# Kernel optimization log

Hardware: AMD Instinct MI355X
Metric: run time of the kernel (lower is better)

## Reference

```python
import jax, jax.numpy as jnp
import numpy as np

M = 28            # mask head resolution (mask_logit[i] is MxM)
NUM_CLASSES = 80  # max value of cls_idx (mask_image channel count)


def setup_inputs() -> dict:
    key = jax.random.key(0)
    k1, k2, k3, k4, k5, k6, k7 = jax.random.split(key, 7)
    N, H, W = 100, 800, 800
    cx = jax.random.uniform(k1, (N,), minval=0.0, maxval=float(W - 1))
    cy = jax.random.uniform(k2, (N,), minval=0.0, maxval=float(H - 1))
    bw = jax.random.uniform(k3, (N,), minval=20.0, maxval=300.0)
    bh = jax.random.uniform(k4, (N,), minval=20.0, maxval=300.0)
    mask_rois = jnp.stack([cx - bw / 2, cy - bh / 2, cx + bw / 2, cy + bh / 2], axis=1).astype(jnp.float32)
    cls_prob = jax.random.uniform(k5, (N,), dtype=jnp.float32)
    mask_prob = jax.random.normal(k6, (N, M, M), dtype=jnp.float32)
    cls_idx = jax.random.randint(k7, (N,), 1, NUM_CLASSES + 1, dtype=jnp.int32)
    return {"mask_rois": mask_rois, "cls_prob": cls_prob, "mask_prob": mask_prob,
            "cls_idx": cls_idx, "im_h": H, "im_w": W}


def _paste(logit, box, H, W):
    """Bilinear-paste an MxM logit into the full HxW image (== cv2.resize to (w,h)
    then placing at the box, evaluated directly on image pixel coords)."""
    x0, y0, x1, y1 = box[0], box[1], box[2], box[3]  # int32
    w = jnp.maximum(x1 - x0 + 1, 1).astype(jnp.float32)
    h = jnp.maximum(y1 - y0 + 1, 1).astype(jnp.float32)
    xs = jnp.arange(W, dtype=jnp.float32)
    ys = jnp.arange(H, dtype=jnp.float32)
    # cv2 bilinear mapping: src = (dst + 0.5) * (M / size) - 0.5, clamped at borders
    sx = jnp.clip((xs - x0.astype(jnp.float32) + 0.5) * (M / w) - 0.5, 0.0, M - 1.0)
    sy = jnp.clip((ys - y0.astype(jnp.float32) + 0.5) * (M / h) - 0.5, 0.0, M - 1.0)
    ix0 = jnp.floor(sx).astype(jnp.int32); ix1 = jnp.minimum(ix0 + 1, M - 1); fx = sx - ix0
    iy0 = jnp.floor(sy).astype(jnp.int32); iy1 = jnp.minimum(iy0 + 1, M - 1); fy = sy - iy0
    v00 = logit[iy0[:, None], ix0[None, :]]
    v01 = logit[iy0[:, None], ix1[None, :]]
    v10 = logit[iy1[:, None], ix0[None, :]]
    v11 = logit[iy1[:, None], ix1[None, :]]
    val = ((1 - fy)[:, None] * ((1 - fx)[None, :] * v00 + fx[None, :] * v01)
           + fy[:, None] * ((1 - fx)[None, :] * v10 + fx[None, :] * v11))
    xi = jnp.arange(W, dtype=jnp.int32)
    yi = jnp.arange(H, dtype=jnp.int32)
    inside_x = (xi >= jnp.maximum(x0, 0)) & (xi < jnp.minimum(x1 + 1, W))
    inside_y = (yi >= jnp.maximum(y0, 0)) & (yi < jnp.minimum(y1 + 1, H))
    inside = inside_y[:, None] & inside_x[None, :]
    return jnp.where(inside, val, 0.0), inside


def _forward(mask_rois, cls_prob, mask_prob, cls_idx, H, W, thr):
    N = mask_prob.shape[0]
    order = jnp.argsort(-cls_prob)                       # sort by score, descending
    boxes = mask_rois[order].astype(jnp.int32)
    logits = mask_prob[order]
    cls = cls_idx[order].astype(jnp.int32) - 1           # 0-based class ids
    pasted, inside = jax.vmap(lambda l, b: _paste(l, b, H, W))(logits, boxes)  # [N,H,W]

    def step(mask_image, xs):
        logit, ins, c = xs
        mask = (logit > 0) & ins                          # thresholded, in-image crop mask
        prev = mask_image[c]
        msum = jnp.sum(mask).astype(jnp.float32)
        ovl = jnp.sum(mask & prev).astype(jnp.float32)    # overlap with accumulated class mask
        keep = (msum > 0) & (ovl <= thr * msum)           # skip if ratio > threshold
        mask_image = mask_image.at[c].set(prev | (mask & keep))
        return mask_image, keep

    mask_image0 = jnp.zeros((NUM_CLASSES, H, W), dtype=bool)
    _, keep = jax.lax.scan(step, mask_image0, (pasted, inside, cls))

    # compact kept masks to the front (frame_id order); dropped boxes go to slot N (discarded)
    pos = jnp.where(keep, jnp.cumsum(keep.astype(jnp.int32)) - 1, N)
    energy = jnp.where(inside & keep[:, None, None], pasted, 0.0)
    full = jnp.zeros((N + 1, H, W), pasted.dtype).at[pos].set(energy)
    mask_energy = full[:N][None]                          # [1, N, H, W], kept masks first
    keep_inds = jnp.full((N + 1,), -1, jnp.int32).at[pos].set(
        jnp.where(keep, order.astype(jnp.int32), -1))[:N]
    return keep_inds, mask_energy


def reference(mask_rois, cls_prob, mask_prob, cls_idx, im_h, im_w):
    return _forward(mask_rois, cls_prob, mask_prob, cls_idx, int(im_h), int(im_w), 0.3)
```

## Files before the change

kernel.cpp:

```cpp
#include <hip/hip_runtime.h>

#define NINST 100
#define MLOG 28
#define IMG 800
#define LOGSZ (MLOG * MLOG)

#define OFF_ORDER 0
#define OFF_CLS   100
#define OFF_BOX   200
#define OFF_MSUM  600
#define OFF_SLOT  800
#define OFF_NK    900
#define OFF_MASK  1024
#define ROWW      12
#define MSTRIDE   (ROWW * 304)
#define PCAP      256
#define F4TOT     (NINST * IMG * IMG / 4)
#define NZBLK     (F4TOT / 256)

__global__ __launch_bounds__(256) void k_mask_zero(const float* __restrict__ mask_prob,
                                                   const float* __restrict__ cls_prob,
                                                   const float* __restrict__ rois,
                                                   const int* __restrict__ cls_idx,
                                                   int* __restrict__ ws,
                                                   float* __restrict__ out) {
    int b = blockIdx.x, tid = threadIdx.x;
    if (b >= NINST) {
        size_t pi = (size_t)(b - NINST) * 256 + tid;
        ((float4*)(out + NINST))[pi] = make_float4(0.f, 0.f, 0.f, 0.f);
        return;
    }
    __shared__ float s_p[NINST];
    __shared__ int s_order[NINST];
    __shared__ float lg[LOGSZ];
    __shared__ int red[256];
    if (tid < NINST) s_p[tid] = cls_prob[tid];
    __syncthreads();
    if (tid < NINST) {
        float p = s_p[tid];
        int r = 0;
        for (int j = 0; j < NINST; j++) {
            float q = s_p[j];
            r += (q > p) || (q == p && j < tid);
        }
        s_order[r] = tid;
    }
    __syncthreads();
    int n = b;
    int orig = s_order[n];
    int x0 = (int)rois[4 * orig], y0 = (int)rois[4 * orig + 1];
    int x1 = (int)rois[4 * orig + 2], y1 = (int)rois[4 * orig + 3];
    if (b == 0 && tid < NINST) {
        int o = s_order[tid];
        ws[OFF_ORDER + tid] = o;
        ws[OFF_CLS + tid] = cls_idx[o] - 1;
#pragma unroll
        for (int k = 0; k < 4; k++)
            ws[OFF_BOX + 4 * tid + k] = (int)rois[4 * o + k];
    }
    for (int i = tid; i < LOGSZ; i += 256) lg[i] = mask_prob[orig * LOGSZ + i];
    __syncthreads();
    int xs = max(x0, 0), xe = min(x1 + 1, IMG);
    int ys = max(y0, 0), ye = min(y1 + 1, IMG);
    int wx0 = xs >> 5, nw = ((xe + 31) >> 5) - wx0, nrows = ye - ys;
    float wf = fmaxf((float)(x1 - x0 + 1), 1.f), hf = fmaxf((float)(y1 - y0 + 1), 1.f);
    float rx = 28.f / wf, ry = 28.f / hf;
    unsigned* mb = (unsigned*)(ws + OFF_MASK) + n * MSTRIDE;
    int total = nrows * nw, cnt = 0;
    for (int t = tid; t < total; t += 256) {
        int row = t / nw, wc = t - row * nw;
        int y = ys + row;
        float sy = ((float)y - (float)y0 + 0.5f) * ry - 0.5f;
        sy = fminf(fmaxf(sy, 0.f), 27.f);
        int iy0 = (int)sy, iy1 = min(iy0 + 1, 27);
        float fy = sy - (float)iy0;
        const float* r0 = lg + iy0 * MLOG;
        const float* r1 = lg + iy1 * MLOG;
        unsigned bits = 0u;
        int xbase = (wx0 + wc) << 5;
        int j0 = max(xs - xbase, 0), j1 = min(xe - xbase, 32);
        for (int j = j0; j < j1; j++) {
            int xx = xbase + j;
            float sx = ((float)xx - (float)x0 + 0.5f) * rx - 0.5f;
            sx = fminf(fmaxf(sx, 0.f), 27.f);
            int ix0 = (int)sx, ix1 = min(ix0 + 1, 27);
            float fx = sx - (float)ix0;
            float val = (1.f - fy) * ((1.f - fx) * r0[ix0] + fx * r0[ix1]) +
                        fy * ((1.f - fx) * r1[ix0] + fx * r1[ix1]);
            bits |= (val > 0.f) ? (1u << j) : 0u;
        }
        mb[row * ROWW + wc] = bits;
        cnt += __popc(bits);
    }
    red[tid] = cnt;
    __syncthreads();
    for (int s = 128; s; s >>= 1) {
        if (tid < s) red[tid] += red[tid + s];
        __syncthreads();
    }
    if (tid == 0) ws[OFF_MSUM + n] = red[0];
}

__device__ __forceinline__ bool box_ovl(const int* sb, int a, int b2) {
    int axs = max(sb[4 * a], 0), axe = min(sb[4 * a + 2] + 1, IMG);
    int ays = max(sb[4 * a + 1], 0), aye = min(sb[4 * a + 3] + 1, IMG);
    int bxs = max(sb[4 * b2], 0), bxe = min(sb[4 * b2 + 2] + 1, IMG);
    int bys = max(sb[4 * b2 + 1], 0), bye = min(sb[4 * b2 + 3] + 1, IMG);
    return axs < bxe && bxs < axe && ays < bye && bys < aye;
}

__global__ __launch_bounds__(64) void k_scan64(int* __restrict__ ws, float* __restrict__ out) {
    int ln = threadIdx.x;
    __shared__ int s_cls[NINST], s_msum[NINST], s_box[4 * NINST];
    __shared__ int s_pi[PCAP], s_pj[PCAP], s_po[PCAP];
    __shared__ int s_np;
    for (int i = ln; i < NINST; i += 64) {
        s_cls[i] = ws[OFF_CLS + i];
        s_msum[i] = ws[OFF_MSUM + i];
    }
    for (int i = ln; i < 4 * NINST; i += 64) s_box[i] = ws[OFF_BOX + i];
    if (ln == 0) s_np = 0;
    const unsigned* maskbase = (const unsigned*)(ws + OFF_MASK);
    __syncthreads();

    for (int i = 0; i < NINST - 1; i++)
        for (int j = i + 1 + ln; j < NINST; j += 64) {
            if (s_cls[i] != s_cls[j] || !s_msum[i] || !s_msum[j]) continue;
            if (!box_ovl(s_box, i, j)) continue;
            int k = atomicAdd(&s_np, 1);
            if (k < PCAP) { s_pi[k] = i; s_pj[k] = j; }
        }
    __syncthreads();
    int np = min(s_np, PCAP);
    bool pov = (s_np > PCAP);
    for (int q = 0; q < np; q++) {
        int i = s_pi[q], j = s_pj[q];
        int ixs = max(s_box[4 * i], 0), ixe = min(s_box[4 * i + 2] + 1, IMG);
        int iys = max(s_box[4 * i + 1], 0);
        int jxs = max(s_box[4 * j], 0), jxe = min(s_box[4 * j + 2] + 1, IMG);
        int jys = max(s_box[4 * j + 1], 0);
        int iye = min(s_box[4 * i + 3] + 1, IMG), jye = min(s_box[4 * j + 3] + 1, IMG);
        int iwx0 = ixs >> 5, jwx0 = jxs >> 5;
        int wlo = max(iwx0, jwx0);
        int whi = min((ixe + 31) >> 5, (jxe + 31) >> 5);
        int rlo = max(iys, jys), rhi = min(iye, jye);
        int nw = whi - wlo, nrows = rhi - rlo;
        const unsigned* mi = maskbase + i * MSTRIDE;
        const unsigned* mj = maskbase + j * MSTRIDE;
        int total = nrows * nw, cnt = 0;
        for (int t = ln; t < total; t += 64) {
            int row = t / nw, wc = t - row * nw;
            int y = rlo + row, w = wlo + wc;
            cnt += __popc(mi[(y - iys) * ROWW + (w - iwx0)] &
                          mj[(y - jys) * ROWW + (w - jwx0)]);
        }
        for (int off = 32; off; off >>= 1) cnt += __shfl_down(cnt, off);
        if (ln == 0) s_po[q] = cnt;
    }
    __syncthreads();

    unsigned long long k0 = 0ull, k1 = 0ull;
    for (int n = 0; n < NINST; n++) {
        int pa = ln, pb = 64 + ln;
        bool ca = (pa < n) && s_cls[pa] == s_cls[n] && ((k0 >> ln) & 1ull) && box_ovl(s_box, pa, n);
        bool cb = (pb < n) && s_cls[pb] == s_cls[n] && ((k1 >> ln) & 1ull) && box_ovl(s_box, pb, n);
        int oa = 0, ob = 0;
        if (!pov) {
            if (ca) for (int q = 0; q < np; q++) if (s_pi[q] == pa && s_pj[q] == n) oa = s_po[q];
            if (cb) for (int q = 0; q < np; q++) if (s_pi[q] == pb && s_pj[q] == n) ob = s_po[q];
        }
        int sum = oa + ob, mx = max(oa, ob);
        for (int off = 32; off; off >>= 1) {
            sum += __shfl_down(sum, off);
            mx = max(mx, __shfl_down(mx, off));
        }
        unsigned long long anyc = __ballot(ca || cb);
        int keep = 0, need = 0;
        if (ln == 0) {
            int msum = s_msum[n];
            float t = 0.3f * (float)msum;
            if (pov) need = (anyc != 0ull) ? 1 : 0, keep = (!need && msum > 0);
            else if ((float)sum <= t) keep = (msum > 0);
            else if ((float)mx > t) keep = 0;
            else need = 1;
        }
        keep = __shfl(keep, 0);
        need = __shfl(need, 0);
        if (need) {
            unsigned long long ba = __ballot(ca), bb = __ballot(cb);
            int nxs = max(s_box[4 * n], 0), nxe = min(s_box[4 * n + 2] + 1, IMG);
            int nys = max(s_box[4 * n + 1], 0), nye = min(s_box[4 * n + 3] + 1, IMG);
            int wx0 = nxs >> 5, nw = ((nxe + 31) >> 5) - wx0, nrows = nye - nys;
            const unsigned* mn = maskbase + n * MSTRIDE;
            int total = nrows * nw, ovl = 0;
            for (int t2 = ln; t2 < total; t2 += 64) {
                int row = t2 / nw, wc = t2 - row * nw;
                unsigned bits = mn[row * ROWW + wc];
                if (!bits) continue;
                int y = nys + row, wa = wx0 + wc;
                unsigned img = 0;
                unsigned long long rem = ba;
                while (rem) {
                    int m = __ffsll((long long)rem) - 1; rem &= rem - 1;
                    int mys = max(s_box[4 * m + 1], 0), mye = min(s_box[4 * m + 3] + 1, IMG);
                    int mxs = max(s_box[4 * m], 0), mxe = min(s_box[4 * m + 2] + 1, IMG);
                    int mwx0 = mxs >> 5, mnw = ((mxe + 31) >> 5) - mwx0;
                    int rr = y - mys, cc = wa - mwx0;
                    if (rr >= 0 && rr < (mye - mys) && cc >= 0 && cc < mnw)
                        img |= maskbase[m * MSTRIDE + rr * ROWW + cc];
                }
                rem = bb;
                while (rem) {
                    int m0 = __ffsll((long long)rem) - 1; rem &= rem - 1;
                    int m = 64 + m0;
                    int mys = max(s_box[4 * m + 1], 0), mye = min(s_box[4 * m + 3] + 1, IMG);
                    int mxs = max(s_box[4 * m], 0), mxe = min(s_box[4 * m + 2] + 1, IMG);
                    int mwx0 = mxs >> 5, mnw = ((mxe + 31) >> 5) - mwx0;
                    int rr = y - mys, cc = wa - mwx0;
                    if (rr >= 0 && rr < (mye - mys) && cc >= 0 && cc < mnw)
                        img |= maskbase[m * MSTRIDE + rr * ROWW + cc];
                }
                ovl += __popc(bits & img);
            }
            for (int off = 32; off; off >>= 1) ovl += __shfl_down(ovl, off);
            if (ln == 0) {
                int msum = s_msum[n];
                keep = (msum > 0) && ((float)ovl <= 0.3f * (float)msum);
            }
            keep = __shfl(keep, 0);
        }
        if (keep) {
            if (n < 64) k0 |= 1ull << n;
            else k1 |= 1ull << (n - 64);
        }
    }

    int nk = __popcll(k0) + __popcll(k1);
    if (ln == 0) ws[OFF_NK] = nk;
    unsigned long long lm = (ln == 0) ? 0ull : (~0ull >> (64 - ln));
    if ((k0 >> ln) & 1ull) {
        int pos = __popcll(k0 & lm);
        ws[OFF_SLOT + pos] = ln;
        out[pos] = (float)ws[OFF_ORDER + ln];
    }
    if (ln < 36 && ((k1 >> ln) & 1ull)) {
        int pos = __popcll(k0) + __popcll(k1 & lm);
        ws[OFF_SLOT + pos] = 64 + ln;
        out[pos] = (float)ws[OFF_ORDER + 64 + ln];
    }
    for (int s = ln; s < NINST; s += 64)
        if (s >= nk) out[s] = -1.f;
}

__global__ __launch_bounds__(256) void k_box(const float* __restrict__ mask_prob,
                                             const int* __restrict__ ws,
                                             float* __restrict__ out) {
    int slot = blockIdx.y, tid = threadIdx.x;
    if (slot >= ws[OFF_NK]) return;
    int n = ws[OFF_SLOT + slot];
    const int* box = ws + OFF_BOX + 4 * n;
    int x0 = box[0], y0 = box[1], x1 = box[2], y1 = box[3];
    int xs = max(x0, 0), xe = min(x1 + 1, IMG);
    int ys = max(y0, 0), ye = min(y1 + 1, IMG);
    int xa = xs & ~3;
    int w4 = (xe - xa + 3) >> 2;
    int rows = ye - ys;
    int total4 = rows * w4;
    __shared__ float lg[LOGSZ];
    int orig = ws[OFF_ORDER + n];
    for (int i = tid; i < LOGSZ; i += 256) lg[i] = mask_prob[orig * LOGSZ + i];
    __syncthreads();
    float wf = fmaxf((float)(x1 - x0 + 1), 1.f), hf = fmaxf((float)(y1 - y0 + 1), 1.f);
    float rx = 28.f / wf, ry = 28.f / hf;
    float* base = out + NINST + (size_t)slot * (IMG * IMG);
    for (int t = blockIdx.x * 256 + tid; t < total4; t += gridDim.x * 256) {
        int row = t / w4, c4 = t - row * w4;
        int y = ys + row, xb = xa + (c4 << 2);
        float sy = ((float)y - (float)y0 + 0.5f) * ry - 0.5f;
        sy = fminf(fmaxf(sy, 0.f), 27.f);
        int iy0 = (int)sy, iy1 = min(iy0 + 1, 27);
        float fy = sy - (float)iy0;
        const float* r0 = lg + iy0 * MLOG;
        const float* r1 = lg + iy1 * MLOG;
        float v[4];
#pragma unroll
        for (int j = 0; j < 4; j++) {
            int xx = xb + j;
            float val = 0.f;
            if (xx >= xs && xx < xe) {
                float sx = ((float)xx - (float)x0 + 0.5f) * rx - 0.5f;
                sx = fminf(fmaxf(sx, 0.f), 27.f);
                int ix0 = (int)sx, ix1 = min(ix0 + 1, 27);
                float fx = sx - (float)ix0;
                val = (1.f - fy) * ((1.f - fx) * r0[ix0] + fx * r0[ix1]) +
                      fy * ((1.f - fx) * r1[ix0] + fx * r1[ix1]);
            }
            v[j] = val;
        }
        *(float4*)(base + (size_t)y * IMG + xb) = make_float4(v[0], v[1], v[2], v[3]);
    }
}

extern "C" void kernel_launch(void* const* d_in, const int* in_sizes, int n_in,
                              void* d_out, int out_size, void* d_ws, size_t ws_size,
                              hipStream_t stream) {
    const float* rois      = (const float*)d_in[0];
    const float* cls_prob  = (const float*)d_in[1];
    const float* mask_prob = (const float*)d_in[2];
    const int*   cls_idx   = (const int*)d_in[3];
    int* ws = (int*)d_ws;
    float* out = (float*)d_out;

    k_mask_zero<<<dim3(NINST + NZBLK), dim3(256), 0, stream>>>(mask_prob, cls_prob, rois, cls_idx, ws, out);
    k_scan64<<<dim3(1), dim3(64), 0, stream>>>(ws, out);
    k_box<<<dim3(91, NINST), dim3(256), 0, stream>>>(mask_prob, ws, out);
}
```

Baseline: 369.5 us.

## Parallelize pairwise mask overlap across blocks and overlap zero-fill with serial scan

Pairwise same-class overlap popcounts move out of the single-wave scan kernel into a new 100x100-block kernel that writes a dense overlap matrix to workspace. The scan kernel then reads that matrix from shared memory, which removes the capped pair list and its overflow fallback. The large output zero-fill moves from the mask kernel into extra blocks of the scan kernel, so the fill runs concurrently with the serial scan. The cost is one more launch, a 40KB shared-memory matrix, and many trivially exiting blocks.

```diff
diff --git a/kernel.cpp b/kernel.cpp
--- a/kernel.cpp
+++ b/kernel.cpp
@@ -11,25 +11,27 @@
 #define OFF_MSUM  600
 #define OFF_SLOT  800
 #define OFF_NK    900
-#define OFF_MASK  1024
+#define OFF_OVL   1024
+#define OFF_MASK  11264
 #define ROWW      12
 #define MSTRIDE   (ROWW * 304)
-#define PCAP      256
 #define F4TOT     (NINST * IMG * IMG / 4)
-#define NZBLK     (F4TOT / 256)
-
-__global__ __launch_bounds__(256) void k_mask_zero(const float* __restrict__ mask_prob,
-                                                   const float* __restrict__ cls_prob,
-                                                   const float* __restrict__ rois,
-                                                   const int* __restrict__ cls_idx,
-                                                   int* __restrict__ ws,
-                                                   float* __restrict__ out) {
+#define NZB       4096
+
+__device__ __forceinline__ bool box_ovl(const int* sb, int a, int b2) {
+    int axs = max(sb[4 * a], 0), axe = min(sb[4 * a + 2] + 1, IMG);
+    int ays = max(sb[4 * a + 1], 0), aye = min(sb[4 * a + 3] + 1, IMG);
+    int bxs = max(sb[4 * b2], 0), bxe = min(sb[4 * b2 + 2] + 1, IMG);
+    int bys = max(sb[4 * b2 + 1], 0), bye = min(sb[4 * b2 + 3] + 1, IMG);
+    return axs < bxe && bxs < axe && ays < bye && bys < aye;
+}
+
+__global__ __launch_bounds__(256) void k_mask(const float* __restrict__ mask_prob,
+                                              const float* __restrict__ cls_prob,
+                                              const float* __restrict__ rois,
+                                              const int* __restrict__ cls_idx,
+                                              int* __restrict__ ws) {
     int b = blockIdx.x, tid = threadIdx.x;
-    if (b >= NINST) {
-        size_t pi = (size_t)(b - NINST) * 256 + tid;
-        ((float4*)(out + NINST))[pi] = make_float4(0.f, 0.f, 0.f, 0.f);
-        return;
-    }
     __shared__ float s_p[NINST];
     __shared__ int s_order[NINST];
     __shared__ float lg[LOGSZ];
@@ -101,86 +103,75 @@
     if (tid == 0) ws[OFF_MSUM + n] = red[0];
 }
 
-__device__ __forceinline__ bool box_ovl(const int* sb, int a, int b2) {
-    int axs = max(sb[4 * a], 0), axe = min(sb[4 * a + 2] + 1, IMG);
-    int ays = max(sb[4 * a + 1], 0), aye = min(sb[4 * a + 3] + 1, IMG);
-    int bxs = max(sb[4 * b2], 0), bxe = min(sb[4 * b2 + 2] + 1, IMG);
-    int bys = max(sb[4 * b2 + 1], 0), bye = min(sb[4 * b2 + 3] + 1, IMG);
-    return axs < bxe && bxs < axe && ays < bye && bys < aye;
-}
-
-__global__ __launch_bounds__(64) void k_scan64(int* __restrict__ ws, float* __restrict__ out) {
-    int ln = threadIdx.x;
+__global__ __launch_bounds__(64) void k_pairs(int* __restrict__ ws) {
+    int i = blockIdx.x, j = blockIdx.y, tid = threadIdx.x;
+    if (i >= j) return;
+    if (ws[OFF_CLS + i] != ws[OFF_CLS + j]) return;
+    if (ws[OFF_MSUM + i] == 0 || ws[OFF_MSUM + j] == 0) return;
+    const int* bi = ws + OFF_BOX + 4 * i;
+    const int* bj = ws + OFF_BOX + 4 * j;
+    int ixs = max(bi[0], 0), ixe = min(bi[2] + 1, IMG);
+    int iys = max(bi[1], 0), iye = min(bi[3] + 1, IMG);
+    int jxs = max(bj[0], 0), jxe = min(bj[2] + 1, IMG);
+    int jys = max(bj[1], 0), jye = min(bj[3] + 1, IMG);
+    if (!(ixs < jxe && jxs < ixe && iys < jye && jys < iye)) return;
+    int iwx0 = ixs >> 5, jwx0 = jxs >> 5;
+    int wlo = max(iwx0, jwx0);
+    int whi = min((ixe + 31) >> 5, (jxe + 31) >> 5);
+    int rlo = max(iys, jys), rhi = min(iye, jye);
+    int nw = whi - wlo, nrows = rhi - rlo;
+    const unsigned* mi = (const unsigned*)(ws + OFF_MASK) + i * MSTRIDE;
+    const unsigned* mj = (const unsigned*)(ws + OFF_MASK) + j * MSTRIDE;
+    int total = nrows * nw, cnt = 0;
+    for (int t = tid; t < total; t += 64) {
+        int row = t / nw, wc = t - row * nw;
+        int y = rlo + row, w = wlo + wc;
+        cnt += __popc(mi[(y - iys) * ROWW + (w - iwx0)] &
+                      mj[(y - jys) * ROWW + (w - jwx0)]);
+    }
+    for (int off = 32; off; off >>= 1) cnt += __shfl_down(cnt, off);
+    if (tid == 0) ws[OFF_OVL + i * NINST + j] = cnt;
+}
+
+__global__ __launch_bounds__(256) void k_scan_zero(int* __restrict__ ws, float* __restrict__ out) {
+    int b = blockIdx.x, tid = threadIdx.x;
+    if (b > 0) {
+        float4* outv = (float4*)(out + NINST);
+        for (size_t pi = (size_t)(b - 1) * 256 + tid; pi < F4TOT; pi += (size_t)NZB * 256)
+            outv[pi] = make_float4(0.f, 0.f, 0.f, 0.f);
+        return;
+    }
+    __shared__ int s_ovl[NINST * NINST];
     __shared__ int s_cls[NINST], s_msum[NINST], s_box[4 * NINST];
-    __shared__ int s_pi[PCAP], s_pj[PCAP], s_po[PCAP];
-    __shared__ int s_np;
-    for (int i = ln; i < NINST; i += 64) {
+    for (int i = tid; i < NINST * NINST; i += 256) s_ovl[i] = ws[OFF_OVL + i];
+    for (int i = tid; i < NINST; i += 256) {
         s_cls[i] = ws[OFF_CLS + i];
         s_msum[i] = ws[OFF_MSUM + i];
     }
-    for (int i = ln; i < 4 * NINST; i += 64) s_box[i] = ws[OFF_BOX + i];
-    if (ln == 0) s_np = 0;
+    for (int i = tid; i < 4 * NINST; i += 256) s_box[i] = ws[OFF_BOX + i];
+    __syncthreads();
+    if (tid >= 64) return;
+    int ln = tid;
     const unsigned* maskbase = (const unsigned*)(ws + OFF_MASK);
-    __syncthreads();
-
-    for (int i = 0; i < NINST - 1; i++)
-        for (int j = i + 1 + ln; j < NINST; j += 64) {
-            if (s_cls[i] != s_cls[j] || !s_msum[i] || !s_msum[j]) continue;
-            if (!box_ovl(s_box, i, j)) continue;
-            int k = atomicAdd(&s_np, 1);
-            if (k < PCAP) { s_pi[k] = i; s_pj[k] = j; }
-        }
-    __syncthreads();
-    int np = min(s_np, PCAP);
-    bool pov = (s_np > PCAP);
-    for (int q = 0; q < np; q++) {
-        int i = s_pi[q], j = s_pj[q];
-        int ixs = max(s_box[4 * i], 0), ixe = min(s_box[4 * i + 2] + 1, IMG);
-        int iys = max(s_box[4 * i + 1], 0);
-        int jxs = max(s_box[4 * j], 0), jxe = min(s_box[4 * j + 2] + 1, IMG);
-        int jys = max(s_box[4 * j + 1], 0);
-        int iye = min(s_box[4 * i + 3] + 1, IMG), jye = min(s_box[4 * j + 3] + 1, IMG);
-        int iwx0 = ixs >> 5, jwx0 = jxs >> 5;
-        int wlo = max(iwx0, jwx0);
-        int whi = min((ixe + 31) >> 5, (jxe + 31) >> 5);
-        int rlo = max(iys, jys), rhi = min(iye, jye);
-        int nw = whi - wlo, nrows = rhi - rlo;
-        const unsigned* mi = maskbase + i * MSTRIDE;
-        const unsigned* mj = maskbase + j * MSTRIDE;
-        int total = nrows * nw, cnt = 0;
-        for (int t = ln; t < total; t += 64) {
-            int row = t / nw, wc = t - row * nw;
-            int y = rlo + row, w = wlo + wc;
-            cnt += __popc(mi[(y - iys) * ROWW + (w - iwx0)] &
-                          mj[(y - jys) * ROWW + (w - jwx0)]);
-        }
-        for (int off = 32; off; off >>= 1) cnt += __shfl_down(cnt, off);
-        if (ln == 0) s_po[q] = cnt;
-    }
-    __syncthreads();
 
     unsigned long long k0 = 0ull, k1 = 0ull;
     for (int n = 0; n < NINST; n++) {
-        int pa = ln, pb = 64 + ln;
-        bool ca = (pa < n) && s_cls[pa] == s_cls[n] && ((k0 >> ln) & 1ull) && box_ovl(s_box, pa, n);
+        int msum = s_msum[n];
+        if (msum == 0) continue;
+        int pb = 64 + ln;
+        bool ca = (ln < n) && s_cls[ln] == s_cls[n] && ((k0 >> ln) & 1ull) && box_ovl(s_box, ln, n);
         bool cb = (pb < n) && s_cls[pb] == s_cls[n] && ((k1 >> ln) & 1ull) && box_ovl(s_box, pb, n);
-        int oa = 0, ob = 0;
-        if (!pov) {
-            if (ca) for (int q = 0; q < np; q++) if (s_pi[q] == pa && s_pj[q] == n) oa = s_po[q];
-            if (cb) for (int q = 0; q < np; q++) if (s_pi[q] == pb && s_pj[q] == n) ob = s_po[q];
-        }
+        int oa = ca ? s_ovl[ln * NINST + n] : 0;
+        int ob = cb ? s_ovl[pb * NINST + n] : 0;
         int sum = oa + ob, mx = max(oa, ob);
         for (int off = 32; off; off >>= 1) {
             sum += __shfl_down(sum, off);
             mx = max(mx, __shfl_down(mx, off));
         }
-        unsigned long long anyc = __ballot(ca || cb);
         int keep = 0, need = 0;
         if (ln == 0) {
-            int msum = s_msum[n];
             float t = 0.3f * (float)msum;
-            if (pov) need = (anyc != 0ull) ? 1 : 0, keep = (!need && msum > 0);
-            else if ((float)sum <= t) keep = (msum > 0);
+            if ((float)sum <= t) keep = 1;
             else if ((float)mx > t) keep = 0;
             else need = 1;
         }
@@ -223,10 +214,7 @@
                 ovl += __popc(bits & img);
             }
             for (int off = 32; off; off >>= 1) ovl += __shfl_down(ovl, off);
-            if (ln == 0) {
-                int msum = s_msum[n];
-                keep = (msum > 0) && ((float)ovl <= 0.3f * (float)msum);
-            }
+            if (ln == 0) keep = ((float)ovl <= 0.3f * (float)msum);
             keep = __shfl(keep, 0);
         }
         if (keep) {
@@ -311,7 +299,8 @@
     int* ws = (int*)d_ws;
     float* out = (float*)d_out;
 
-    k_mask_zero<<<dim3(NINST + NZBLK), dim3(256), 0, stream>>>(mask_prob, cls_prob, rois, cls_idx, ws, out);
-    k_scan64<<<dim3(1), dim3(64), 0, stream>>>(ws, out);
+    k_mask<<<dim3(NINST), dim3(256), 0, stream>>>(mask_prob, cls_prob, rois, cls_idx, ws);
+    k_pairs<<<dim3(NINST, NINST), dim3(64), 0, stream>>>(ws);
+    k_scan_zero<<<dim3(NZB + 1), dim3(256), 0, stream>>>(ws, out);
     k_box<<<dim3(91, NINST), dim3(256), 0, stream>>>(mask_prob, ws, out);
 }
```

Result: faster. 357.1 us (-3.4%).
